# Performance work log

Measured on AMD Instinct MI355X. Metric: run time of the kernel, lower is better.

Reference implementation:

```python
import jax, jax.numpy as jnp
import numpy as np

MARGIN = 0.2
ALPHA = 2.0
BETA = 1.5
ANGLE_THRESHOLD = 30.0
EPS_PD = 1e-6   # F.pairwise_distance eps
EPS_CS = 1e-8   # F.cosine_similarity eps
NEG_INF = -1e30
POS_INF = 1e30


def setup_inputs() -> dict:
    key = jax.random.key(0)
    k1, k2, k3 = jax.random.split(key, 3)
    B, F, A = 4096, 512, 3
    features = jax.random.normal(k1, (B, F), dtype=jnp.float32)
    labels = jax.random.randint(k2, (B,), 0, 256)
    angles = jax.random.uniform(k3, (B, A), dtype=jnp.float32) * 90.0  # degrees
    features_orig = jax.random.normal(jax.random.fold_in(key, 7), (B, F), dtype=jnp.float32)
    return {"features": features, "labels": labels, "angles": angles, "features_orig": features_orig}


def _cosine_sim_matrix(f):
    norms = jnp.linalg.norm(f, axis=1)
    denom = jnp.maximum(norms[:, None] * norms[None, :], EPS_CS)
    return (f @ f.T) / denom


def _forward(features, labels, angles, features_orig):
    B = features.shape[0]
    idx = jnp.arange(B)
    # pairwise angle distances [B,B] (torch.cdist p=2)
    adist = jnp.sqrt(jnp.sum((angles[:, None, :] - angles[None, :, :]) ** 2, axis=-1))
    same = labels[:, None] == labels[None, :]
    same = same & ~jnp.eye(B, dtype=bool)          # exclude self
    diff = labels[:, None] != labels[None, :]
    has_pos = same.any(axis=1)
    has_neg = diff.any(axis=1)
    valid = has_pos & has_neg
    # hardest positive: same label, largest angle difference
    pos_idx = jnp.argmax(jnp.where(same, adist, NEG_INF), axis=1)
    # hardest negative: among diff-label within angle threshold, most similar feature;
    # else diff-label with smallest angle difference
    sim = _cosine_sim_matrix(features)
    similar = diff & (adist < ANGLE_THRESHOLD)
    sim_any = similar.any(axis=1)
    neg_idx_hard = jnp.argmax(jnp.where(similar, sim, NEG_INF), axis=1)
    neg_idx_far = jnp.argmin(jnp.where(diff, adist, POS_INF), axis=1)
    neg_idx = jnp.where(sim_any, neg_idx_hard, neg_idx_far)
    # triplet distances (F.pairwise_distance adds eps to the diff)
    a = features
    p = features[pos_idx]
    n = features[neg_idx]
    pos_d = jnp.linalg.norm(a - p + EPS_PD, axis=1)
    neg_d = jnp.linalg.norm(a - n + EPS_PD, axis=1)
    # angle-based weights (non-differentiable, matches .item() in torch)
    pa = adist[idx, pos_idx]
    na = adist[idx, neg_idx]
    w = jnp.where(pa > 45.0, ALPHA, 1.0) * jnp.where(na < 15.0, BETA, 1.0)
    basic = jax.nn.relu(pos_d - neg_d + MARGIN)
    vmask = valid.astype(features.dtype)
    cnt = jnp.maximum(vmask.sum(), 1.0)
    triplet_loss = jnp.sum(w * basic * vmask) / cnt
    # reconstruction term
    num = jnp.sum(features * features_orig, axis=1)
    den = jnp.maximum(jnp.linalg.norm(features, axis=1) * jnp.linalg.norm(features_orig, axis=1), EPS_CS)
    recon = 1.0 - jnp.mean(num / den)
    return triplet_loss + 0.1 * recon


def reference(features, labels, angles, features_orig):
    return _forward(features, labels, angles, features_orig)
```

## Files before the change

kernel.cpp:

```cpp
#include <hip/hip_runtime.h>
#include <math.h>

#define BN 4096
#define FD 512
#define TT 128
#define TJ 64
#define BK 64
#define NJT (BN / TT)
#define NPAIR (NJT * (NJT + 1) / 2)
#define NBLK (NPAIR * 2)
#define NPC 128

typedef __attribute__((ext_vector_type(8))) __bf16 bf16x8;
typedef __attribute__((ext_vector_type(4))) float floatx4;
typedef unsigned long long u64;

__device__ __forceinline__ float wred_sum(float v) {
#pragma unroll
  for (int m = 1; m < 64; m <<= 1) v += __shfl_xor(v, m, 64);
  return v;
}

__device__ __forceinline__ float dot4(float4 a, float4 b) {
  return a.x * b.x + a.y * b.y + a.z * b.z + a.w * b.w;
}

__device__ __forceinline__ unsigned short f2bf(float x) {
  unsigned u = __float_as_uint(x);
  u += 0x7fffu + ((u >> 16) & 1u);
  return (unsigned short)(u >> 16);
}

__device__ __forceinline__ void load16(const void* g, void* l) {
  __builtin_amdgcn_global_load_lds(
      (const __attribute__((address_space(1))) unsigned int*)g,
      (__attribute__((address_space(3))) unsigned int*)l, 16, 0, 0);
}

__device__ __forceinline__ unsigned ford(float v) {
  unsigned u = __float_as_uint(v);
  return u ^ (((unsigned)((int)u >> 31)) | 0x80000000u);
}

template <int N>
__device__ __forceinline__ int rori(int x) {
  return __builtin_amdgcn_update_dpp(0, x, 0x120 | N, 0xf, 0xf, true);
}
template <int N>
__device__ __forceinline__ u64 ror16_u64(u64 k) {
  unsigned lo = (unsigned)rori<N>((int)(unsigned)k);
  unsigned hi = (unsigned)rori<N>((int)(unsigned)(k >> 32));
  return ((u64)hi << 32) | lo;
}
__device__ __forceinline__ u64 red16_max_u64(u64 k) {
  u64 o;
  o = ror16_u64<1>(k); k = o > k ? o : k;
  o = ror16_u64<2>(k); k = o > k ? o : k;
  o = ror16_u64<4>(k); k = o > k ? o : k;
  o = ror16_u64<8>(k); k = o > k ? o : k;
  return k;
}

__device__ __forceinline__ u64 sx64(u64 v, int m) {
  unsigned lo = (unsigned)__shfl_xor((int)(unsigned)v, m, 64);
  unsigned hi = (unsigned)__shfl_xor((int)(unsigned)(v >> 32), m, 64);
  return ((u64)hi << 32) | lo;
}

__global__ __launch_bounds__(256) void k_prep(const float* __restrict__ f,
                                              const float* __restrict__ fo,
                                              const float* __restrict__ angles,
                                              unsigned short* __restrict__ gb,
                                              float* __restrict__ rowr,
                                              float* __restrict__ ax,
                                              float* __restrict__ ay,
                                              float* __restrict__ az) {
  const int i = blockIdx.x * 4 + (threadIdx.x >> 6);
  const int lane = threadIdx.x & 63;
  const int t = blockIdx.x * 256 + threadIdx.x;
  if (t < BN) {
    ax[t] = angles[t * 3 + 0];
    ay[t] = angles[t * 3 + 1];
    az[t] = angles[t * 3 + 2];
  }
  const float4* fr = (const float4*)(f + (size_t)i * FD);
  const float4* orr = (const float4*)(fo + (size_t)i * FD);
  float4 x0 = fr[lane], x1 = fr[lane + 64];
  float4 y0 = orr[lane], y1 = orr[lane + 64];
  float sff = dot4(x0, x0) + dot4(x1, x1);
  float sfo = dot4(x0, y0) + dot4(x1, y1);
  float soo = dot4(y0, y0) + dot4(y1, y1);
  sff = wred_sum(sff);
  sfo = wred_sum(sfo);
  soo = wred_sum(soo);
  float nf = sqrtf(sff);
  float inv = 1.0f / nf;
  ushort4* gr = (ushort4*)(gb + (size_t)i * FD);
  ushort4 s0, s1;
  s0.x = f2bf(x0.x * inv); s0.y = f2bf(x0.y * inv);
  s0.z = f2bf(x0.z * inv); s0.w = f2bf(x0.w * inv);
  s1.x = f2bf(x1.x * inv); s1.y = f2bf(x1.y * inv);
  s1.z = f2bf(x1.z * inv); s1.w = f2bf(x1.w * inv);
  gr[lane] = s0;
  gr[lane + 64] = s1;
  if (lane == 0) {
    rowr[i] = sfo / fmaxf(nf * sqrtf(soo), 1e-8f);
  }
}

__global__ __launch_bounds__(256) void k_sim(const unsigned short* __restrict__ gb,
                                             const int* __restrict__ labels,
                                             const float* __restrict__ ax,
                                             const float* __restrict__ ay,
                                             const float* __restrict__ az,
                                             u64* __restrict__ pkey) {
  __shared__ unsigned short As[TT * BK];
  __shared__ unsigned short Bs[TJ * BK];
  const int h = blockIdx.x & 1;
  int a = 0, rem = blockIdx.x >> 1;
#pragma unroll 1
  while (rem >= NJT - a) { rem -= NJT - a; a++; }
  const int b = a + rem;
  const int i0 = a * TT;
  const int j0 = b * TT + h * TJ;

  const int tid = threadIdx.x;
  const int w = tid >> 6;
  const int lane = tid & 63;

  floatx4 acc[2][4];
#pragma unroll
  for (int u = 0; u < 2; u++)
#pragma unroll
    for (int v = 0; v < 4; v++) acc[u][v] = (floatx4){0.f, 0.f, 0.f, 0.f};

  const int rp = tid >> 3;
  const int q8 = ((tid & 7) ^ (rp & 7)) * 8;
  const unsigned short* gA[4];
  const unsigned short* gB[2];
  unsigned short* lA[4];
  unsigned short* lB[2];
#pragma unroll
  for (int c = 0; c < 4; c++) {
    gA[c] = gb + (size_t)(i0 + rp + 32 * c) * FD + q8;
    lA[c] = As + (tid + 256 * c) * 8;
  }
#pragma unroll
  for (int c = 0; c < 2; c++) {
    gB[c] = gb + (size_t)(j0 + rp + 32 * c) * FD + q8;
    lB[c] = Bs + (tid + 256 * c) * 8;
  }

  const int m = lane & 15;
  const int arow = w * 32 + m;
  const int brow = m;
  const int g4 = lane >> 4;
  const int l7 = lane & 7;
  const int koff0 = (g4 ^ l7) * 8;
  const int koff1 = ((4 + g4) ^ l7) * 8;

  for (int kc = 0; kc < FD; kc += BK) {
#pragma unroll
    for (int c = 0; c < 4; c++) load16(gA[c] + kc, lA[c]);
#pragma unroll
    for (int c = 0; c < 2; c++) load16(gB[c] + kc, lB[c]);
    __syncthreads();
    bf16x8 af[2], bf[4];
#pragma unroll
    for (int u = 0; u < 2; u++)
      af[u] = *(const bf16x8*)(As + (arow + u * 16) * BK + koff0);
#pragma unroll
    for (int v = 0; v < 4; v++)
      bf[v] = *(const bf16x8*)(Bs + (brow + v * 16) * BK + koff0);
#pragma unroll
    for (int u = 0; u < 2; u++)
#pragma unroll
      for (int v = 0; v < 4; v++)
        acc[u][v] = __builtin_amdgcn_mfma_f32_16x16x32_bf16(af[u], bf[v], acc[u][v], 0, 0, 0);
#pragma unroll
    for (int u = 0; u < 2; u++)
      af[u] = *(const bf16x8*)(As + (arow + u * 16) * BK + koff1);
#pragma unroll
    for (int v = 0; v < 4; v++)
      bf[v] = *(const bf16x8*)(Bs + (brow + v * 16) * BK + koff1);
#pragma unroll
    for (int u = 0; u < 2; u++)
#pragma unroll
      for (int v = 0; v < 4; v++)
        acc[u][v] = __builtin_amdgcn_mfma_f32_16x16x32_bf16(af[u], bf[v], acc[u][v], 0, 0, 0);
    __syncthreads();
  }

  const int quad = lane >> 4;
  const int cx = lane & 15;
  int jc[4], lj[4];
  float jx[4], jy[4], jz[4];
#pragma unroll
  for (int v = 0; v < 4; v++) {
    jc[v] = j0 + v * 16 + cx;
    lj[v] = labels[jc[v]];
    jx[v] = ax[jc[v]];
    jy[v] = ay[jc[v]];
    jz[v] = az[jc[v]];
  }
  const size_t rbase = (size_t)(64 + 2 * b + h) * BN;
  u64 ckey[4] = {0, 0, 0, 0};
#pragma unroll
  for (int u = 0; u < 2; u++) {
#pragma unroll
    for (int reg = 0; reg < 4; reg++) {
      int i = i0 + w * 32 + u * 16 + quad * 4 + reg;
      int li = labels[i];
      float a0 = ax[i], a1 = ay[i], a2 = az[i];
      u64 rkey = 0;
      unsigned ni = (unsigned)(~i);
#pragma unroll
      for (int v = 0; v < 4; v++) {
        float d0 = a0 - jx[v];
        float d1 = a1 - jy[v];
        float d2 = a2 - jz[v];
        float dd = d0 * d0 + d1 * d1 + d2 * d2;
        bool ok = (li != lj[v]) && (dd < 900.0f);
        u64 vh = (u64)ford(acc[u][v][reg]) << 32;
        u64 candR = vh | (unsigned)(~jc[v]);
        if (ok && candR > rkey) rkey = candR;
        u64 candC = vh | ni;
        if (ok && candC > ckey[v]) ckey[v] = candC;
      }
      rkey = red16_max_u64(rkey);
      if (cx == 0) pkey[rbase + i] = rkey;
    }
  }
  if (a != b) {
    const size_t cbase = (size_t)(4 * a + w) * BN;
#pragma unroll
    for (int v = 0; v < 4; v++) {
      u64 k = ckey[v];
      u64 o = sx64(k, 16); if (o > k) k = o;
      o = sx64(k, 32); if (o > k) k = o;
      if (quad == 0) pkey[cbase + jc[v]] = k;
    }
  }
}

__global__ __launch_bounds__(256) void k_final(const float* __restrict__ f,
                                               const int* __restrict__ labels,
                                               const float* __restrict__ ax,
                                               const float* __restrict__ ay,
                                               const float* __restrict__ az,
                                               const u64* __restrict__ pkey,
                                               float* __restrict__ rowc,
                                               float* __restrict__ rowv) {
  const int i = blockIdx.x * 4 + (threadIdx.x >> 6);
  const int lane = threadIdx.x & 63;
  const int li = labels[i];
  const float a0 = ax[i], a1 = ay[i], a2 = az[i];

  u64 keyP = 0;
  u64 keyN = ~0ull;
  const float4* ax4 = (const float4*)ax;
  const float4* ay4 = (const float4*)ay;
  const float4* az4 = (const float4*)az;
  const int4* lb4 = (const int4*)labels;
#pragma unroll
  for (int it = 0; it < 16; it++) {
    int bb = it * 64 + lane;
    float4 X = ax4[bb], Y = ay4[bb], Z = az4[bb];
    int4 L = lb4[bb];
    int jb = bb * 4;
#pragma unroll
    for (int s = 0; s < 4; s++) {
      float xx = s == 0 ? X.x : s == 1 ? X.y : s == 2 ? X.z : X.w;
      float yy = s == 0 ? Y.x : s == 1 ? Y.y : s == 2 ? Y.z : Y.w;
      float zz = s == 0 ? Z.x : s == 1 ? Z.y : s == 2 ? Z.z : Z.w;
      int ll = s == 0 ? L.x : s == 1 ? L.y : s == 2 ? L.z : L.w;
      int j = jb + s;
      float d0 = a0 - xx, d1 = a1 - yy, d2 = a2 - zz;
      float dd = d0 * d0 + d1 * d1 + d2 * d2;
      if (ll == li) {
        u64 kp = ((u64)__float_as_uint(dd) << 32) | (unsigned)(~j);
        if (j != i && kp > keyP) keyP = kp;
      } else {
        u64 kn = ((u64)__float_as_uint(dd) << 32) | (unsigned)j;
        if (kn < keyN) keyN = kn;
      }
    }
  }
  const int t = i >> 7;
  u64 s0 = (lane < 4 * t) ? pkey[(size_t)lane * BN + i] : 0;
  u64 s1 = (lane >= 2 * t) ? pkey[(size_t)(64 + lane) * BN + i] : 0;
  u64 keyS = s0 > s1 ? s0 : s1;
#pragma unroll
  for (int off = 1; off < 64; off <<= 1) {
    u64 o = sx64(keyP, off);
    if (o > keyP) keyP = o;
    o = sx64(keyN, off);
    if (o < keyN) keyN = o;
    o = sx64(keyS, off);
    if (o > keyS) keyS = o;
  }
  bool hp = keyP != 0;
  bool hn = keyN != ~0ull;
  if (!(hp && hn)) {
    if (lane == 0) { rowc[i] = 0.0f; rowv[i] = 0.0f; }
    return;
  }
  bool sim_any = keyS != 0;
  int pos = (int)(~(unsigned)keyP);
  int neg = sim_any ? (int)(~(unsigned)keyS) : (int)(unsigned)keyN;

  const float4* fa = (const float4*)(f + (size_t)i * FD);
  const float4* fp = (const float4*)(f + (size_t)pos * FD);
  const float4* fn = (const float4*)(f + (size_t)neg * FD);
  float sp = 0.0f, sn = 0.0f;
#pragma unroll
  for (int t2 = 0; t2 < 2; t2++) {
    float4 xa = fa[lane + t2 * 64];
    float4 xp = fp[lane + t2 * 64];
    float4 xn = fn[lane + t2 * 64];
    float dp;
    dp = xa.x - xp.x + 1e-6f; sp += dp * dp;
    dp = xa.y - xp.y + 1e-6f; sp += dp * dp;
    dp = xa.z - xp.z + 1e-6f; sp += dp * dp;
    dp = xa.w - xp.w + 1e-6f; sp += dp * dp;
    dp = xa.x - xn.x + 1e-6f; sn += dp * dp;
    dp = xa.y - xn.y + 1e-6f; sn += dp * dp;
    dp = xa.z - xn.z + 1e-6f; sn += dp * dp;
    dp = xa.w - xn.w + 1e-6f; sn += dp * dp;
  }
  sp = wred_sum(sp);
  sn = wred_sum(sn);

  if (lane == 0) {
    float pos_d = sqrtf(sp);
    float neg_d = sqrtf(sn);
    float pa = sqrtf(__uint_as_float((unsigned)(keyP >> 32)));
    float n0 = a0 - ax[neg];
    float n1 = a1 - ay[neg];
    float n2 = a2 - az[neg];
    float na = sqrtf(n0 * n0 + n1 * n1 + n2 * n2);
    float w = (pa > 45.0f ? 2.0f : 1.0f) * (na < 15.0f ? 1.5f : 1.0f);
    float basic = fmaxf(pos_d - neg_d + 0.2f, 0.0f);
    rowc[i] = w * basic;
    rowv[i] = 1.0f;
  }
}

__global__ __launch_bounds__(1024) void k_out(const float* __restrict__ rowc,
                                              const float* __restrict__ rowv,
                                              const float* __restrict__ rowr,
                                              float* __restrict__ out) {
  __shared__ float sc[16], sv[16], sr[16];
  const int t = threadIdx.x;
  float c = 0.0f, v = 0.0f, r = 0.0f;
  for (int i = t; i < BN; i += 1024) {
    c += rowc[i];
    v += rowv[i];
    r += rowr[i];
  }
  c = wred_sum(c);
  v = wred_sum(v);
  r = wred_sum(r);
  const int wid = t >> 6;
  if ((t & 63) == 0) { sc[wid] = c; sv[wid] = v; sr[wid] = r; }
  __syncthreads();
  if (t == 0) {
    float C = 0.0f, V = 0.0f, R = 0.0f;
#pragma unroll
    for (int k = 0; k < 16; k++) { C += sc[k]; V += sv[k]; R += sr[k]; }
    float tri = C / fmaxf(V, 1.0f);
    float recon = 1.0f - R / (float)BN;
    out[0] = tri + 0.1f * recon;
  }
}

extern "C" void kernel_launch(void* const* d_in, const int* in_sizes, int n_in,
                              void* d_out, int out_size, void* d_ws, size_t ws_size,
                              hipStream_t stream) {
  const float* feat = (const float*)d_in[0];
  const int* labels = (const int*)d_in[1];
  const float* angles = (const float*)d_in[2];
  const float* forig = (const float*)d_in[3];
  float* out = (float*)d_out;

  char* ws = (char*)d_ws;
  unsigned short* gb = (unsigned short*)ws;
  size_t off = (size_t)BN * FD * sizeof(unsigned short);
  u64* pkey = (u64*)(ws + off);     off += (size_t)NPC * BN * 8;
  float* rowc = (float*)(ws + off); off += (size_t)BN * 4;
  float* rowv = (float*)(ws + off); off += (size_t)BN * 4;
  float* rowr = (float*)(ws + off); off += (size_t)BN * 4;
  float* ax = (float*)(ws + off);   off += (size_t)BN * 4;
  float* ay = (float*)(ws + off);   off += (size_t)BN * 4;
  float* az = (float*)(ws + off);   off += (size_t)BN * 4;

  k_prep<<<BN / 4, 256, 0, stream>>>(feat, forig, angles, gb, rowr, ax, ay, az);
  k_sim<<<NBLK, 256, 0, stream>>>(gb, labels, ax, ay, az, pkey);
  k_final<<<BN / 4, 256, 0, stream>>>(feat, labels, ax, ay, az, pkey, rowc, rowv);
  k_out<<<1, 1024, 0, stream>>>(rowc, rowv, rowr, out);
}
```

Before: 108.9 us.

## Load A fragments directly from global in k_sim and stage angles in LDS in k_final

In the similarity kernel, the A tile is no longer staged through shared memory. Each wave reads its own MFMA A fragments straight from global memory into registers, which removes the A LDS stores and reads and cuts LDS use. In the final kernel, angle and label vectors are loaded cooperatively into shared memory in chunks, so each wave reads them from LDS instead of every wave rereading them from global. The risk is that uncoalesced 16-byte global reads per lane for A and the extra barriers in k_final may cost more than the LDS traffic they replace.

Result: slower. 117.9 us (+8.2%).

```diff
diff --git a/kernel.cpp b/kernel.cpp
--- a/kernel.cpp
+++ b/kernel.cpp
@@ -114,7 +114,6 @@
                                              const float* __restrict__ ay,
                                              const float* __restrict__ az,
                                              u64* __restrict__ pkey) {
-  __shared__ unsigned short As[TT * BK];
   __shared__ unsigned short Bs[TJ * BK];
   const int h = blockIdx.x & 1;
   int a = 0, rem = blockIdx.x >> 1;
@@ -136,15 +135,8 @@
 
   const int rp = tid >> 3;
   const int q8 = ((tid & 7) ^ (rp & 7)) * 8;
-  const unsigned short* gA[4];
   const unsigned short* gB[2];
-  unsigned short* lA[4];
   unsigned short* lB[2];
-#pragma unroll
-  for (int c = 0; c < 4; c++) {
-    gA[c] = gb + (size_t)(i0 + rp + 32 * c) * FD + q8;
-    lA[c] = As + (tid + 256 * c) * 8;
-  }
 #pragma unroll
   for (int c = 0; c < 2; c++) {
     gB[c] = gb + (size_t)(j0 + rp + 32 * c) * FD + q8;
@@ -152,23 +144,24 @@
   }
 
   const int m = lane & 15;
-  const int arow = w * 32 + m;
-  const int brow = m;
   const int g4 = lane >> 4;
   const int l7 = lane & 7;
   const int koff0 = (g4 ^ l7) * 8;
   const int koff1 = ((4 + g4) ^ l7) * 8;
+  const int brow = m;
+  const unsigned short* gA0 = gb + (size_t)(i0 + w * 32 + m) * FD + g4 * 8;
 
   for (int kc = 0; kc < FD; kc += BK) {
-#pragma unroll
-    for (int c = 0; c < 4; c++) load16(gA[c] + kc, lA[c]);
-#pragma unroll
-    for (int c = 0; c < 2; c++) load16(gB[c] + kc, lB[c]);
+    load16(gB[0] + kc, lB[0]);
+    load16(gB[1] + kc, lB[1]);
+    bf16x8 af0[2], af1[2];
+#pragma unroll
+    for (int u = 0; u < 2; u++) {
+      af0[u] = *(const bf16x8*)(gA0 + (size_t)u * 16 * FD + kc);
+      af1[u] = *(const bf16x8*)(gA0 + (size_t)u * 16 * FD + kc + 32);
+    }
     __syncthreads();
-    bf16x8 af[2], bf[4];
-#pragma unroll
-    for (int u = 0; u < 2; u++)
-      af[u] = *(const bf16x8*)(As + (arow + u * 16) * BK + koff0);
+    bf16x8 bf[4];
 #pragma unroll
     for (int v = 0; v < 4; v++)
       bf[v] = *(const bf16x8*)(Bs + (brow + v * 16) * BK + koff0);
@@ -176,10 +169,7 @@
     for (int u = 0; u < 2; u++)
 #pragma unroll
       for (int v = 0; v < 4; v++)
-        acc[u][v] = __builtin_amdgcn_mfma_f32_16x16x32_bf16(af[u], bf[v], acc[u][v], 0, 0, 0);
-#pragma unroll
-    for (int u = 0; u < 2; u++)
-      af[u] = *(const bf16x8*)(As + (arow + u * 16) * BK + koff1);
+        acc[u][v] = __builtin_amdgcn_mfma_f32_16x16x32_bf16(af0[u], bf[v], acc[u][v], 0, 0, 0);
 #pragma unroll
     for (int v = 0; v < 4; v++)
       bf[v] = *(const bf16x8*)(Bs + (brow + v * 16) * BK + koff1);
@@ -187,7 +177,7 @@
     for (int u = 0; u < 2; u++)
 #pragma unroll
       for (int v = 0; v < 4; v++)
-        acc[u][v] = __builtin_amdgcn_mfma_f32_16x16x32_bf16(af[u], bf[v], acc[u][v], 0, 0, 0);
+        acc[u][v] = __builtin_amdgcn_mfma_f32_16x16x32_bf16(af1[u], bf[v], acc[u][v], 0, 0, 0);
     __syncthreads();
   }
 
@@ -251,8 +241,11 @@
                                                const u64* __restrict__ pkey,
                                                float* __restrict__ rowc,
                                                float* __restrict__ rowv) {
+  __shared__ float4 sax[256], say[256], saz[256];
+  __shared__ int4 slb[256];
   const int i = blockIdx.x * 4 + (threadIdx.x >> 6);
   const int lane = threadIdx.x & 63;
+  const int tid = threadIdx.x;
   const int li = labels[i];
   const float a0 = ax[i], a1 = ay[i], a2 = az[i];
 
@@ -262,29 +255,38 @@
   const float4* ay4 = (const float4*)ay;
   const float4* az4 = (const float4*)az;
   const int4* lb4 = (const int4*)labels;
-#pragma unroll
-  for (int it = 0; it < 16; it++) {
-    int bb = it * 64 + lane;
-    float4 X = ax4[bb], Y = ay4[bb], Z = az4[bb];
-    int4 L = lb4[bb];
-    int jb = bb * 4;
-#pragma unroll
-    for (int s = 0; s < 4; s++) {
-      float xx = s == 0 ? X.x : s == 1 ? X.y : s == 2 ? X.z : X.w;
-      float yy = s == 0 ? Y.x : s == 1 ? Y.y : s == 2 ? Y.z : Y.w;
-      float zz = s == 0 ? Z.x : s == 1 ? Z.y : s == 2 ? Z.z : Z.w;
-      int ll = s == 0 ? L.x : s == 1 ? L.y : s == 2 ? L.z : L.w;
-      int j = jb + s;
-      float d0 = a0 - xx, d1 = a1 - yy, d2 = a2 - zz;
-      float dd = d0 * d0 + d1 * d1 + d2 * d2;
-      if (ll == li) {
-        u64 kp = ((u64)__float_as_uint(dd) << 32) | (unsigned)(~j);
-        if (j != i && kp > keyP) keyP = kp;
-      } else {
-        u64 kn = ((u64)__float_as_uint(dd) << 32) | (unsigned)j;
-        if (kn < keyN) keyN = kn;
+#pragma unroll 1
+  for (int r = 0; r < 4; r++) {
+    sax[tid] = ax4[r * 256 + tid];
+    say[tid] = ay4[r * 256 + tid];
+    saz[tid] = az4[r * 256 + tid];
+    slb[tid] = lb4[r * 256 + tid];
+    __syncthreads();
+#pragma unroll
+    for (int it = 0; it < 4; it++) {
+      int idx = it * 64 + lane;
+      float4 X = sax[idx], Y = say[idx], Z = saz[idx];
+      int4 L = slb[idx];
+      int jb = (r * 256 + idx) * 4;
+#pragma unroll
+      for (int s = 0; s < 4; s++) {
+        float xx = s == 0 ? X.x : s == 1 ? X.y : s == 2 ? X.z : X.w;
+        float yy = s == 0 ? Y.x : s == 1 ? Y.y : s == 2 ? Y.z : Y.w;
+        float zz = s == 0 ? Z.x : s == 1 ? Z.y : s == 2 ? Z.z : Z.w;
+        int ll = s == 0 ? L.x : s == 1 ? L.y : s == 2 ? L.z : L.w;
+        int j = jb + s;
+        float d0 = a0 - xx, d1 = a1 - yy, d2 = a2 - zz;
+        float dd = d0 * d0 + d1 * d1 + d2 * d2;
+        if (ll == li) {
+          u64 kp = ((u64)__float_as_uint(dd) << 32) | (unsigned)(~j);
+          if (j != i && kp > keyP) keyP = kp;
+        } else {
+          u64 kn = ((u64)__float_as_uint(dd) << 32) | (unsigned)j;
+          if (kn < keyN) keyN = kn;
+        }
       }
     }
+    __syncthreads();
   }
   const int t = i >> 7;
   u64 s0 = (lane < 4 * t) ? pkey[(size_t)lane * BN + i] : 0;
```
